# Kernel optimization log

Hardware: AMD Instinct MI355X
Metric: run time of the kernel (lower is better)

The kernel has to match this reference:

```python
import jax, jax.numpy as jnp
import numpy as np

N = 10000      # nodes
E = 320000     # edges
IN_DIM = 256
HID = 256
EDGE_DIM = 64


def _sage(x, src, dst, w_l, b_l, w_r, n_nodes):
    """PyG SAGEConv (aggr='mean', root_weight=True, normalize=False):
    out_i = lin_l(mean_{j->i} x_j) + lin_r(x_i). Messages flow src->dst."""
    msg = x[src]                                            # [E, F]
    agg = jax.ops.segment_sum(msg, dst, num_segments=n_nodes)
    cnt = jax.ops.segment_sum(jnp.ones((msg.shape[0], 1), x.dtype), dst,
                              num_segments=n_nodes)
    mean = agg / jnp.maximum(cnt, 1.0)                      # [N, F]
    return mean @ w_l.T + b_l + x @ w_r.T                   # [N, HID]


def setup_inputs() -> dict:
    key = jax.random.key(0)
    ks = jax.random.split(key, 13)
    s = 0.02
    return {
        "x": jax.random.normal(ks[0], (N, IN_DIM), dtype=jnp.float32),
        "edge_attr": jax.random.normal(ks[1], (E, EDGE_DIM), dtype=jnp.float32),
        "conv1_wl": jax.random.normal(ks[2], (HID, IN_DIM), dtype=jnp.float32) * s,
        "conv1_bl": jnp.zeros((HID,), dtype=jnp.float32),
        "conv1_wr": jax.random.normal(ks[3], (HID, IN_DIM), dtype=jnp.float32) * s,
        "conv2_wl": jax.random.normal(ks[4], (HID, HID), dtype=jnp.float32) * s,
        "conv2_bl": jnp.zeros((HID,), dtype=jnp.float32),
        "conv2_wr": jax.random.normal(ks[5], (HID, HID), dtype=jnp.float32) * s,
        "mlp_w1": jax.random.normal(ks[6], (HID, 2 * HID + EDGE_DIM), dtype=jnp.float32) * s,
        "mlp_b1": jnp.zeros((HID,), dtype=jnp.float32),
        "mlp_w2": jax.random.normal(ks[7], (1, HID), dtype=jnp.float32) * s,
        "mlp_b2": jnp.zeros((1,), dtype=jnp.float32),
        "edge_index": jax.random.randint(ks[8], (2, E), 0, N, dtype=jnp.int32),
    }


def reference(x, edge_attr, conv1_wl, conv1_bl, conv1_wr,
              conv2_wl, conv2_bl, conv2_wr,
              mlp_w1, mlp_b1, mlp_w2, mlp_b2, edge_index):
    src, dst = edge_index[0], edge_index[1]
    # encode_nodes (dropout is identity in eval mode)
    h = jax.nn.relu(_sage(x, src, dst, conv1_wl, conv1_bl, conv1_wr, N))
    h = _sage(h, src, dst, conv2_wl, conv2_bl, conv2_wr, N)
    # edge_logits: gather endpoints, concat with edge_attr, 2-layer MLP
    feats = jnp.concatenate([h[src], h[dst], edge_attr], axis=1)   # [E, 2H+ED]
    hidden = jax.nn.relu(feats @ mlp_w1.T + mlp_b1)                # [E, H]
    logits = hidden @ mlp_w2.T + mlp_b2                            # [E, 1]
    return logits[:, 0]
```

## Files before the change

### kernel.cpp

```cpp
#include <hip/hip_runtime.h>

#define N_NODES 10000
#define N_EDGES 320000
#define DIM 256
#define ED 64
#define W1_LD 576

__global__ void hist_kernel(const int* __restrict__ dst, int* __restrict__ cnt, int n) {
  int i = blockIdx.x * blockDim.x + threadIdx.x;
  if (i < n) atomicAdd(&cnt[dst[i]], 1);
}

__global__ void scan_kernel(const int* __restrict__ cnt, int* __restrict__ off,
                            int* __restrict__ cursor, int n) {
  __shared__ int wsum[4];
  __shared__ int carry_s;
  int t = threadIdx.x, lane = t & 63, w = t >> 6;
  if (t == 0) carry_s = 0;
  __syncthreads();
  for (int base = 0; base < n; base += 256) {
    int i = base + t;
    int v = (i < n) ? cnt[i] : 0;
    int sc = v;
    #pragma unroll
    for (int s = 1; s < 64; s <<= 1) {
      int u = __shfl_up(sc, s, 64);
      if (lane >= s) sc += u;
    }
    if (lane == 63) wsum[w] = sc;
    __syncthreads();
    int woff = 0, tot = 0;
    #pragma unroll
    for (int j = 0; j < 4; ++j) { int s = wsum[j]; if (j < w) woff += s; tot += s; }
    int excl = sc - v + woff + carry_s;
    if (i < n) { off[i] = excl; cursor[i] = excl; }
    __syncthreads();
    if (t == 0) carry_s += tot;
    __syncthreads();
  }
  if (t == 0) off[n] = carry_s;
}

__global__ void scatter_kernel(const int* __restrict__ src, const int* __restrict__ dst,
                               int* __restrict__ cursor, int* __restrict__ csr_src, int n) {
  int i = blockIdx.x * blockDim.x + threadIdx.x;
  if (i < n) {
    int p = atomicAdd(&cursor[dst[i]], 1);
    csr_src[p] = src[i];
  }
}

__global__ __launch_bounds__(256) void aggregate_kernel(
    const float* __restrict__ X, const int* __restrict__ off,
    const int* __restrict__ csr_src, float* __restrict__ out) {
  int node = blockIdx.x * 4 + (threadIdx.x >> 6);
  int t4 = (threadIdx.x & 63) * 4;
  int beg = off[node], end = off[node + 1];
  float x0=0.f,y0=0.f,z0=0.f,w0=0.f, x1=0.f,y1=0.f,z1=0.f,w1=0.f;
  float x2=0.f,y2=0.f,z2=0.f,w2=0.f, x3=0.f,y3=0.f,z3=0.f,w3=0.f;
  int e = beg;
  for (; e + 3 < end; e += 4) {
    int s0 = csr_src[e], s1 = csr_src[e+1], s2 = csr_src[e+2], s3 = csr_src[e+3];
    float4 v0 = *(const float4*)&X[(size_t)s0 * DIM + t4];
    float4 v1 = *(const float4*)&X[(size_t)s1 * DIM + t4];
    float4 v2 = *(const float4*)&X[(size_t)s2 * DIM + t4];
    float4 v3 = *(const float4*)&X[(size_t)s3 * DIM + t4];
    x0+=v0.x; y0+=v0.y; z0+=v0.z; w0+=v0.w;
    x1+=v1.x; y1+=v1.y; z1+=v1.z; w1+=v1.w;
    x2+=v2.x; y2+=v2.y; z2+=v2.z; w2+=v2.w;
    x3+=v3.x; y3+=v3.y; z3+=v3.z; w3+=v3.w;
  }
  for (; e < end; ++e) {
    int s = csr_src[e];
    float4 v = *(const float4*)&X[(size_t)s * DIM + t4];
    x0+=v.x; y0+=v.y; z0+=v.z; w0+=v.w;
  }
  int deg = end - beg;
  float inv = 1.0f / (float)(deg > 0 ? deg : 1);
  float4 r;
  r.x = (x0+x1+x2+x3) * inv; r.y = (y0+y1+y2+y3) * inv;
  r.z = (z0+z1+z2+z3) * inv; r.w = (w0+w1+w2+w3) * inv;
  *(float4*)&out[(size_t)node * DIM + t4] = r;
}

template<bool SECOND, bool RELU>
__global__ __launch_bounds__(256) void gemm_kernel(
    const float* __restrict__ W1_, const float* __restrict__ A1,
    const float* __restrict__ A2, const float* __restrict__ W2_,
    const float* __restrict__ bias, float* __restrict__ C,
    int nrows, int K, int ldw, int ldc, int wsplit) {
  __shared__ float As[32][128];
  __shared__ float Bs[32][64];
  int t = threadIdx.x;
  int tx = t & 15, ty = t >> 4;
  int row0 = blockIdx.x * 128;
  int col0 = blockIdx.y * 64;

  const float* W1 = W1_;
  const float* W2 = W2_;
  bool qreg = (col0 >= wsplit);
  if (qreg) {
    ptrdiff_t adj = (ptrdiff_t)wsplit - (ptrdiff_t)wsplit * (ptrdiff_t)ldw;
    W1 = W1_ + adj; W2 = W2_ + adj;
  }

  float acc[8][4];
  #pragma unroll
  for (int i = 0; i < 8; ++i)
    #pragma unroll
    for (int j = 0; j < 4; ++j) acc[i][j] = 0.f;

  int ksteps = K / 32;
  int total = SECOND ? 2 * ksteps : ksteps;
  for (int kt = 0; kt < total; ++kt) {
    bool second = SECOND && (kt >= ksteps);
    const float* A = second ? A2 : A1;
    const float* W = second ? W2 : W1;
    int kb = (second ? (kt - ksteps) : kt) * 32;
    __syncthreads();
    #pragma unroll
    for (int i = 0; i < 4; ++i) {
      int idx = i * 256 + t;
      int m = idx >> 3;
      int kq = idx & 7;
      int row = row0 + m;
      float4 v = make_float4(0.f, 0.f, 0.f, 0.f);
      if (row < nrows) v = *(const float4*)&A[(size_t)row * K + kb + kq * 4];
      As[kq * 4 + 0][m] = v.x; As[kq * 4 + 1][m] = v.y;
      As[kq * 4 + 2][m] = v.z; As[kq * 4 + 3][m] = v.w;
    }
    #pragma unroll
    for (int i = 0; i < 2; ++i) {
      int idx = i * 256 + t;
      int o = idx >> 3;
      int kq = idx & 7;
      float4 v = *(const float4*)&W[(size_t)(col0 + o) * ldw + kb + kq * 4];
      Bs[kq * 4 + 0][o] = v.x; Bs[kq * 4 + 1][o] = v.y;
      Bs[kq * 4 + 2][o] = v.z; Bs[kq * 4 + 3][o] = v.w;
    }
    __syncthreads();
    #pragma unroll 8
    for (int k = 0; k < 32; ++k) {
      float4 a0 = *(const float4*)&As[k][ty * 4];
      float4 a1 = *(const float4*)&As[k][ty * 4 + 64];
      float4 b0 = *(const float4*)&Bs[k][tx * 4];
      float a[8] = {a0.x, a0.y, a0.z, a0.w, a1.x, a1.y, a1.z, a1.w};
      float b[4] = {b0.x, b0.y, b0.z, b0.w};
      #pragma unroll
      for (int i = 0; i < 8; ++i)
        #pragma unroll
        for (int j = 0; j < 4; ++j)
          acc[i][j] += a[i] * b[j];
    }
  }
  float4 bv = make_float4(0.f, 0.f, 0.f, 0.f);
  if (bias && !qreg) bv = *(const float4*)&bias[col0 + tx * 4];
  #pragma unroll
  for (int i = 0; i < 8; ++i) {
    int m = ty * 4 + (i & 3) + (i >> 2) * 64;
    int row = row0 + m;
    if (row < nrows) {
      float4 o4;
      o4.x = acc[i][0] + bv.x; o4.y = acc[i][1] + bv.y;
      o4.z = acc[i][2] + bv.z; o4.w = acc[i][3] + bv.w;
      if (RELU) {
        o4.x = fmaxf(o4.x, 0.f); o4.y = fmaxf(o4.y, 0.f);
        o4.z = fmaxf(o4.z, 0.f); o4.w = fmaxf(o4.w, 0.f);
      }
      *(float4*)&C[(size_t)row * ldc + col0 + tx * 4] = o4;
    }
  }
}

#define EB 64
__global__ __launch_bounds__(256) void edge_kernel(
    const float* __restrict__ edge_attr,
    const int* __restrict__ src, const int* __restrict__ dst,
    const float* __restrict__ PQ,
    const float* __restrict__ mlp_w1,
    const float* __restrict__ w2,
    const float* __restrict__ b2,
    float* __restrict__ out) {
  __shared__ float w_lds[64][128];
  __shared__ float ea_lds[64][EB];
  __shared__ int sid[2][EB];

  int t = threadIdx.x;
  int e0 = blockIdx.x * EB;
  if (t < EB) { sid[0][t] = src[e0 + t]; sid[1][t] = dst[e0 + t]; }
  {
    int e_l = t >> 2, q = t & 3;
    const float* ep = &edge_attr[(size_t)(e0 + e_l) * ED + q * 16];
    #pragma unroll
    for (int j = 0; j < 4; ++j) {
      float4 v = *(const float4*)&ep[j * 4];
      int k = q * 16 + j * 4;
      ea_lds[k + 0][e_l] = v.x; ea_lds[k + 1][e_l] = v.y;
      ea_lds[k + 2][e_l] = v.z; ea_lds[k + 3][e_l] = v.w;
    }
  }
  int c = t & 15, r = t >> 4;
  float logit[4] = {0.f, 0.f, 0.f, 0.f};
  __syncthreads();

  const float* pbase[4];
  const float* qbase[4];
  #pragma unroll
  for (int i = 0; i < 4; ++i) {
    int el = r * 4 + i;
    pbase[i] = &PQ[(size_t)sid[0][el] * 512 + c * 4];
    qbase[i] = &PQ[(size_t)sid[1][el] * 512 + 256 + c * 4];
  }

  float4 pf[4][2], qf[4][2];
  #pragma unroll
  for (int i = 0; i < 4; ++i) {
    pf[i][0] = *(const float4*)&pbase[i][0];
    pf[i][1] = *(const float4*)&pbase[i][64];
    qf[i][0] = *(const float4*)&qbase[i][0];
    qf[i][1] = *(const float4*)&qbase[i][64];
  }

  for (int half = 0; half < 2; ++half) {
    #pragma unroll
    for (int i = 0; i < 8; ++i) {
      int idx = i * 256 + t;
      int o = idx & 127;
      int kq = idx >> 7;
      float4 v = *(const float4*)&mlp_w1[(size_t)(half * 128 + o) * W1_LD + 512 + kq * 4];
      w_lds[kq * 4 + 0][o] = v.x; w_lds[kq * 4 + 1][o] = v.y;
      w_lds[kq * 4 + 2][o] = v.z; w_lds[kq * 4 + 3][o] = v.w;
    }
    __syncthreads();
    float acc[4][8];
    #pragma unroll
    for (int i = 0; i < 4; ++i)
      #pragma unroll
      for (int j = 0; j < 8; ++j) acc[i][j] = 0.f;
    #pragma unroll 8
    for (int k = 0; k < 64; ++k) {
      float4 a = *(const float4*)&ea_lds[k][r * 4];
      float4 wv0 = *(const float4*)&w_lds[k][c * 4];
      float4 wv1 = *(const float4*)&w_lds[k][c * 4 + 64];
      float av[4] = {a.x, a.y, a.z, a.w};
      float wv[8] = {wv0.x, wv0.y, wv0.z, wv0.w, wv1.x, wv1.y, wv1.z, wv1.w};
      #pragma unroll
      for (int i = 0; i < 4; ++i)
        #pragma unroll
        for (int j = 0; j < 8; ++j)
          acc[i][j] += av[i] * wv[j];
    }
    float4 w2a = *(const float4*)&w2[half * 128 + c * 4];
    float4 w2b = *(const float4*)&w2[half * 128 + c * 4 + 64];
    float w2v[8] = {w2a.x, w2a.y, w2a.z, w2a.w, w2b.x, w2b.y, w2b.z, w2b.w};
    #pragma unroll
    for (int i = 0; i < 4; ++i) {
      float pv[8] = {pf[i][0].x, pf[i][0].y, pf[i][0].z, pf[i][0].w,
                     pf[i][1].x, pf[i][1].y, pf[i][1].z, pf[i][1].w};
      float qv[8] = {qf[i][0].x, qf[i][0].y, qf[i][0].z, qf[i][0].w,
                     qf[i][1].x, qf[i][1].y, qf[i][1].z, qf[i][1].w};
      #pragma unroll
      for (int j = 0; j < 8; ++j) {
        float s = acc[i][j] + pv[j] + qv[j];
        s = fmaxf(s, 0.f);
        logit[i] += s * w2v[j];
      }
    }
    if (half == 0) {
      #pragma unroll
      for (int i = 0; i < 4; ++i) {
        pf[i][0] = *(const float4*)&pbase[i][128];
        pf[i][1] = *(const float4*)&pbase[i][192];
        qf[i][0] = *(const float4*)&qbase[i][128];
        qf[i][1] = *(const float4*)&qbase[i][192];
      }
      __syncthreads();
    }
  }
  #pragma unroll
  for (int m = 1; m < 16; m <<= 1) {
    #pragma unroll
    for (int i = 0; i < 4; ++i) logit[i] += __shfl_xor(logit[i], m, 64);
  }
  if (c == 0) {
    float bb = b2[0];
    #pragma unroll
    for (int i = 0; i < 4; ++i) out[e0 + r * 4 + i] = logit[i] + bb;
  }
}

static inline size_t alignup(size_t x) { return (x + 255) & ~(size_t)255; }

extern "C" void kernel_launch(void* const* d_in, const int* in_sizes, int n_in,
                              void* d_out, int out_size, void* d_ws, size_t ws_size,
                              hipStream_t stream) {
  const float* x    = (const float*)d_in[0];
  const float* ea   = (const float*)d_in[1];
  const float* c1wl = (const float*)d_in[2];
  const float* c1bl = (const float*)d_in[3];
  const float* c1wr = (const float*)d_in[4];
  const float* c2wl = (const float*)d_in[5];
  const float* c2bl = (const float*)d_in[6];
  const float* c2wr = (const float*)d_in[7];
  const float* w1   = (const float*)d_in[8];
  const float* b1   = (const float*)d_in[9];
  const float* w2   = (const float*)d_in[10];
  const float* b2   = (const float*)d_in[11];
  const int*   ei   = (const int*)d_in[12];
  const int* src = ei;
  const int* dst = ei + N_EDGES;
  float* out = (float*)d_out;

  char* p = (char*)d_ws;
  size_t o = 0;
  int* cnt      = (int*)(p + o); o += alignup(N_NODES * 4);
  int* off      = (int*)(p + o); o += alignup((N_NODES + 1) * 4);
  int* cursor   = (int*)(p + o); o += alignup(N_NODES * 4);
  int* csr_src  = (int*)(p + o); o += alignup(N_EDGES * 4);
  float* mbuf   = (float*)(p + o); o += alignup((size_t)N_NODES * DIM * 4);
  float* h1     = (float*)(p + o); o += alignup((size_t)N_NODES * DIM * 4);
  float* h2     = (float*)(p + o); o += alignup((size_t)N_NODES * DIM * 4);
  float* PQ     = (float*)(p + o); o += alignup((size_t)N_NODES * 512 * 4);

  hipMemsetAsync(cnt, 0, N_NODES * 4, stream);
  hist_kernel<<<(N_EDGES + 255) / 256, 256, 0, stream>>>(dst, cnt, N_EDGES);
  scan_kernel<<<1, 256, 0, stream>>>(cnt, off, cursor, N_NODES);
  scatter_kernel<<<(N_EDGES + 255) / 256, 256, 0, stream>>>(src, dst, cursor, csr_src, N_EDGES);

  dim3 ggrid((N_NODES + 127) / 128, 4);
  dim3 pqgrid((N_NODES + 127) / 128, 8);
  const int NOSPLIT = 1 << 30;

  aggregate_kernel<<<N_NODES / 4, 256, 0, stream>>>(x, off, csr_src, mbuf);
  gemm_kernel<true, true><<<ggrid, 256, 0, stream>>>(
      c1wl, mbuf, x, c1wr, c1bl, h1, N_NODES, DIM, DIM, DIM, NOSPLIT);

  aggregate_kernel<<<N_NODES / 4, 256, 0, stream>>>(h1, off, csr_src, mbuf);
  gemm_kernel<true, false><<<ggrid, 256, 0, stream>>>(
      c2wl, mbuf, h1, c2wr, c2bl, h2, N_NODES, DIM, DIM, DIM, NOSPLIT);

  gemm_kernel<false, false><<<pqgrid, 256, 0, stream>>>(
      w1, h2, h2, w1, b1, PQ, N_NODES, DIM, W1_LD, 512, 256);

  edge_kernel<<<N_EDGES / EB, 256, 0, stream>>>(ea, src, dst, PQ, w1, w2, b2, out);
}
```

Baseline: 663.9 us.

## Process edges in dst-sorted CSR order and shrink GEMM and edge tiles

The scatter kernel now also records the destination and original edge id for each CSR slot. The edge kernel walks edges in destination-sorted order, so the Q-half rows of PQ are reused across neighbouring edges and gathers get better cache locality. Logits are written back through the stored edge id, and edge_attr reads become indirect. GEMM tiles shrink from 128 to 64 rows and the edge kernel's weight tile from 128 to 64 columns, with a launch-bounds hint, to raise occupancy and block count; the cost is lower per-thread reuse and more W1 reloads.

```diff
diff --git a/kernel.cpp b/kernel.cpp
--- a/kernel.cpp
+++ b/kernel.cpp
@@ -42,11 +42,15 @@
 }
 
 __global__ void scatter_kernel(const int* __restrict__ src, const int* __restrict__ dst,
-                               int* __restrict__ cursor, int* __restrict__ csr_src, int n) {
+                               int* __restrict__ cursor, int* __restrict__ csr_src,
+                               int* __restrict__ csr_dst, int* __restrict__ csr_eid, int n) {
   int i = blockIdx.x * blockDim.x + threadIdx.x;
   if (i < n) {
-    int p = atomicAdd(&cursor[dst[i]], 1);
+    int d = dst[i];
+    int p = atomicAdd(&cursor[d], 1);
     csr_src[p] = src[i];
+    csr_dst[p] = d;
+    csr_eid[p] = i;
   }
 }
 
@@ -89,11 +93,11 @@
     const float* __restrict__ A2, const float* __restrict__ W2_,
     const float* __restrict__ bias, float* __restrict__ C,
     int nrows, int K, int ldw, int ldc, int wsplit) {
-  __shared__ float As[32][128];
+  __shared__ float As[32][64];
   __shared__ float Bs[32][64];
   int t = threadIdx.x;
   int tx = t & 15, ty = t >> 4;
-  int row0 = blockIdx.x * 128;
+  int row0 = blockIdx.x * 64;
   int col0 = blockIdx.y * 64;
 
   const float* W1 = W1_;
@@ -104,9 +108,9 @@
     W1 = W1_ + adj; W2 = W2_ + adj;
   }
 
-  float acc[8][4];
-  #pragma unroll
-  for (int i = 0; i < 8; ++i)
+  float acc[4][4];
+  #pragma unroll
+  for (int i = 0; i < 4; ++i)
     #pragma unroll
     for (int j = 0; j < 4; ++j) acc[i][j] = 0.f;
 
@@ -119,7 +123,7 @@
     int kb = (second ? (kt - ksteps) : kt) * 32;
     __syncthreads();
     #pragma unroll
-    for (int i = 0; i < 4; ++i) {
+    for (int i = 0; i < 2; ++i) {
       int idx = i * 256 + t;
       int m = idx >> 3;
       int kq = idx & 7;
@@ -142,12 +146,11 @@
     #pragma unroll 8
     for (int k = 0; k < 32; ++k) {
       float4 a0 = *(const float4*)&As[k][ty * 4];
-      float4 a1 = *(const float4*)&As[k][ty * 4 + 64];
       float4 b0 = *(const float4*)&Bs[k][tx * 4];
-      float a[8] = {a0.x, a0.y, a0.z, a0.w, a1.x, a1.y, a1.z, a1.w};
+      float a[4] = {a0.x, a0.y, a0.z, a0.w};
       float b[4] = {b0.x, b0.y, b0.z, b0.w};
       #pragma unroll
-      for (int i = 0; i < 8; ++i)
+      for (int i = 0; i < 4; ++i)
         #pragma unroll
         for (int j = 0; j < 4; ++j)
           acc[i][j] += a[i] * b[j];
@@ -156,9 +159,8 @@
   float4 bv = make_float4(0.f, 0.f, 0.f, 0.f);
   if (bias && !qreg) bv = *(const float4*)&bias[col0 + tx * 4];
   #pragma unroll
-  for (int i = 0; i < 8; ++i) {
-    int m = ty * 4 + (i & 3) + (i >> 2) * 64;
-    int row = row0 + m;
+  for (int i = 0; i < 4; ++i) {
+    int row = row0 + ty * 4 + i;
     if (row < nrows) {
       float4 o4;
       o4.x = acc[i][0] + bv.x; o4.y = acc[i][1] + bv.y;
@@ -173,24 +175,24 @@
 }
 
 #define EB 64
-__global__ __launch_bounds__(256) void edge_kernel(
+__global__ __launch_bounds__(256, 4) void edge_kernel(
     const float* __restrict__ edge_attr,
-    const int* __restrict__ src, const int* __restrict__ dst,
+    const int* __restrict__ csr_src, const int* __restrict__ csr_dst,
+    const int* __restrict__ csr_eid,
     const float* __restrict__ PQ,
     const float* __restrict__ mlp_w1,
     const float* __restrict__ w2,
     const float* __restrict__ b2,
     float* __restrict__ out) {
-  __shared__ float w_lds[64][128];
+  __shared__ float w_lds[64][64];
   __shared__ float ea_lds[64][EB];
-  __shared__ int sid[2][EB];
 
   int t = threadIdx.x;
   int e0 = blockIdx.x * EB;
-  if (t < EB) { sid[0][t] = src[e0 + t]; sid[1][t] = dst[e0 + t]; }
   {
     int e_l = t >> 2, q = t & 3;
-    const float* ep = &edge_attr[(size_t)(e0 + e_l) * ED + q * 16];
+    int eid = csr_eid[e0 + e_l];
+    const float* ep = &edge_attr[(size_t)eid * ED + q * 16];
     #pragma unroll
     for (int j = 0; j < 4; ++j) {
       float4 v = *(const float4*)&ep[j * 4];
@@ -200,79 +202,67 @@
     }
   }
   int c = t & 15, r = t >> 4;
-  float logit[4] = {0.f, 0.f, 0.f, 0.f};
-  __syncthreads();
-
   const float* pbase[4];
   const float* qbase[4];
+  int eout[4];
   #pragma unroll
   for (int i = 0; i < 4; ++i) {
-    int el = r * 4 + i;
-    pbase[i] = &PQ[(size_t)sid[0][el] * 512 + c * 4];
-    qbase[i] = &PQ[(size_t)sid[1][el] * 512 + 256 + c * 4];
-  }
-
-  float4 pf[4][2], qf[4][2];
+    int el = e0 + r * 4 + i;
+    pbase[i] = &PQ[(size_t)csr_src[el] * 512 + c * 4];
+    qbase[i] = &PQ[(size_t)csr_dst[el] * 512 + 256 + c * 4];
+    eout[i] = csr_eid[el];
+  }
+  float logit[4] = {0.f, 0.f, 0.f, 0.f};
+  float4 pf[4], qf[4];
   #pragma unroll
   for (int i = 0; i < 4; ++i) {
-    pf[i][0] = *(const float4*)&pbase[i][0];
-    pf[i][1] = *(const float4*)&pbase[i][64];
-    qf[i][0] = *(const float4*)&qbase[i][0];
-    qf[i][1] = *(const float4*)&qbase[i][64];
-  }
-
-  for (int half = 0; half < 2; ++half) {
-    #pragma unroll
-    for (int i = 0; i < 8; ++i) {
+    pf[i] = *(const float4*)&pbase[i][0];
+    qf[i] = *(const float4*)&qbase[i][0];
+  }
+
+  for (int chunk = 0; chunk < 4; ++chunk) {
+    #pragma unroll
+    for (int i = 0; i < 4; ++i) {
       int idx = i * 256 + t;
-      int o = idx & 127;
-      int kq = idx >> 7;
-      float4 v = *(const float4*)&mlp_w1[(size_t)(half * 128 + o) * W1_LD + 512 + kq * 4];
+      int o = idx & 63;
+      int kq = idx >> 6;
+      float4 v = *(const float4*)&mlp_w1[(size_t)(chunk * 64 + o) * W1_LD + 512 + kq * 4];
       w_lds[kq * 4 + 0][o] = v.x; w_lds[kq * 4 + 1][o] = v.y;
       w_lds[kq * 4 + 2][o] = v.z; w_lds[kq * 4 + 3][o] = v.w;
     }
     __syncthreads();
-    float acc[4][8];
+    float acc[4][4];
     #pragma unroll
     for (int i = 0; i < 4; ++i)
       #pragma unroll
-      for (int j = 0; j < 8; ++j) acc[i][j] = 0.f;
+      for (int j = 0; j < 4; ++j) acc[i][j] = 0.f;
     #pragma unroll 8
     for (int k = 0; k < 64; ++k) {
       float4 a = *(const float4*)&ea_lds[k][r * 4];
-      float4 wv0 = *(const float4*)&w_lds[k][c * 4];
-      float4 wv1 = *(const float4*)&w_lds[k][c * 4 + 64];
+      float4 wv4 = *(const float4*)&w_lds[k][c * 4];
       float av[4] = {a.x, a.y, a.z, a.w};
-      float wv[8] = {wv0.x, wv0.y, wv0.z, wv0.w, wv1.x, wv1.y, wv1.z, wv1.w};
+      float wv[4] = {wv4.x, wv4.y, wv4.z, wv4.w};
       #pragma unroll
       for (int i = 0; i < 4; ++i)
         #pragma unroll
-        for (int j = 0; j < 8; ++j)
+        for (int j = 0; j < 4; ++j)
           acc[i][j] += av[i] * wv[j];
     }
-    float4 w2a = *(const float4*)&w2[half * 128 + c * 4];
-    float4 w2b = *(const float4*)&w2[half * 128 + c * 4 + 64];
-    float w2v[8] = {w2a.x, w2a.y, w2a.z, w2a.w, w2b.x, w2b.y, w2b.z, w2b.w};
+    float4 w2v = *(const float4*)&w2[chunk * 64 + c * 4];
     #pragma unroll
     for (int i = 0; i < 4; ++i) {
-      float pv[8] = {pf[i][0].x, pf[i][0].y, pf[i][0].z, pf[i][0].w,
-                     pf[i][1].x, pf[i][1].y, pf[i][1].z, pf[i][1].w};
-      float qv[8] = {qf[i][0].x, qf[i][0].y, qf[i][0].z, qf[i][0].w,
-                     qf[i][1].x, qf[i][1].y, qf[i][1].z, qf[i][1].w};
-      #pragma unroll
-      for (int j = 0; j < 8; ++j) {
-        float s = acc[i][j] + pv[j] + qv[j];
-        s = fmaxf(s, 0.f);
-        logit[i] += s * w2v[j];
-      }
-    }
-    if (half == 0) {
+      float s0 = fmaxf(acc[i][0] + pf[i].x + qf[i].x, 0.f);
+      float s1 = fmaxf(acc[i][1] + pf[i].y + qf[i].y, 0.f);
+      float s2 = fmaxf(acc[i][2] + pf[i].z + qf[i].z, 0.f);
+      float s3 = fmaxf(acc[i][3] + pf[i].w + qf[i].w, 0.f);
+      logit[i] += s0 * w2v.x + s1 * w2v.y + s2 * w2v.z + s3 * w2v.w;
+    }
+    if (chunk < 3) {
+      int coff = (chunk + 1) * 64;
       #pragma unroll
       for (int i = 0; i < 4; ++i) {
-        pf[i][0] = *(const float4*)&pbase[i][128];
-        pf[i][1] = *(const float4*)&pbase[i][192];
-        qf[i][0] = *(const float4*)&qbase[i][128];
-        qf[i][1] = *(const float4*)&qbase[i][192];
+        pf[i] = *(const float4*)&pbase[i][coff];
+        qf[i] = *(const float4*)&qbase[i][coff];
       }
       __syncthreads();
     }
@@ -285,7 +275,7 @@
   if (c == 0) {
     float bb = b2[0];
     #pragma unroll
-    for (int i = 0; i < 4; ++i) out[e0 + r * 4 + i] = logit[i] + bb;
+    for (int i = 0; i < 4; ++i) out[eout[i]] = logit[i] + bb;
   }
 }
 
@@ -317,6 +307,8 @@
   int* off      = (int*)(p + o); o += alignup((N_NODES + 1) * 4);
   int* cursor   = (int*)(p + o); o += alignup(N_NODES * 4);
   int* csr_src  = (int*)(p + o); o += alignup(N_EDGES * 4);
+  int* csr_dst  = (int*)(p + o); o += alignup(N_EDGES * 4);
+  int* csr_eid  = (int*)(p + o); o += alignup(N_EDGES * 4);
   float* mbuf   = (float*)(p + o); o += alignup((size_t)N_NODES * DIM * 4);
   float* h1     = (float*)(p + o); o += alignup((size_t)N_NODES * DIM * 4);
   float* h2     = (float*)(p + o); o += alignup((size_t)N_NODES * DIM * 4);
@@ -325,10 +317,11 @@
   hipMemsetAsync(cnt, 0, N_NODES * 4, stream);
   hist_kernel<<<(N_EDGES + 255) / 256, 256, 0, stream>>>(dst, cnt, N_EDGES);
   scan_kernel<<<1, 256, 0, stream>>>(cnt, off, cursor, N_NODES);
-  scatter_kernel<<<(N_EDGES + 255) / 256, 256, 0, stream>>>(src, dst, cursor, csr_src, N_EDGES);
-
-  dim3 ggrid((N_NODES + 127) / 128, 4);
-  dim3 pqgrid((N_NODES + 127) / 128, 8);
+  scatter_kernel<<<(N_EDGES + 255) / 256, 256, 0, stream>>>(
+      src, dst, cursor, csr_src, csr_dst, csr_eid, N_EDGES);
+
+  dim3 ggrid((N_NODES + 63) / 64, 4);
+  dim3 pqgrid((N_NODES + 63) / 64, 8);
   const int NOSPLIT = 1 << 30;
 
   aggregate_kernel<<<N_NODES / 4, 256, 0, stream>>>(x, off, csr_src, mbuf);
@@ -342,5 +335,6 @@
   gemm_kernel<false, false><<<pqgrid, 256, 0, stream>>>(
       w1, h2, h2, w1, b1, PQ, N_NODES, DIM, W1_LD, 512, 256);
 
-  edge_kernel<<<N_EDGES / EB, 256, 0, stream>>>(ea, src, dst, PQ, w1, w2, b2, out);
-}
+  edge_kernel<<<N_EDGES / EB, 256, 0, stream>>>(
+      ea, csr_src, csr_dst, csr_eid, PQ, w1, w2, b2, out);
+}
```

New measurement: 616.4 us. -7.2%, faster.
